# Optimization experiments

Measured on AMD Instinct MI355X. Metric: run time of the kernel, lower is better.

The kernel has to match this reference:

```python
import jax, jax.numpy as jnp
import numpy as np
import math

B, N, HID, NH = 128, 512, 512, 8
DH = HID // NH  # d_heads = 64


def setup_inputs() -> dict:
    key = jax.random.key(0)
    ks = jax.random.split(key, 8)
    s = 0.05  # keep logits in a sane range
    h = jax.random.normal(ks[0], (B, N, HID), dtype=jnp.float32)
    lengths = jax.random.randint(ks[1], (B,), 1, N + 1, dtype=jnp.int32)
    w_q = jax.random.normal(ks[2], (HID, HID), dtype=jnp.float32) * s
    w_k = jax.random.normal(ks[3], (HID, HID), dtype=jnp.float32) * s
    w_v = jax.random.normal(ks[4], (HID, HID), dtype=jnp.float32) * s
    w_o = jax.random.normal(ks[5], (HID, HID), dtype=jnp.float32) * s
    w_seed_w = jax.random.normal(ks[6], (HID, 1), dtype=jnp.float32) * s  # Linear(1, k*hidden), k=1
    w_seed_b = jax.random.normal(ks[7], (HID,), dtype=jnp.float32) * s
    seed_vec = jnp.ones((1,), dtype=jnp.float32)
    return {"h": h, "lengths": lengths, "w_q": w_q, "w_k": w_k, "w_v": w_v,
            "w_o": w_o, "w_seed_w": w_seed_w, "w_seed_b": w_seed_b, "seed_vec": seed_vec}


def reference(h, lengths, w_q, w_k, w_v, w_o, w_seed_w, w_seed_b, seed_vec):
    # PMA with k=1 seed query. norm_features=False.
    # query = w_seed(seed_vec), same for every graph in the batch.
    query = w_seed_w @ seed_vec + w_seed_b            # [HID]
    q = (w_q @ query).reshape(NH, DH)                 # [NH, DH] (Linear: x @ W.T == W @ x for vector)
    # NOTE: original code computes w_k(v) but never uses it in attention; output
    # depends only on q and v (e = q * v summed over d_heads). We skip the dead compute.
    v = (h @ w_v.T).reshape(B, N, NH, DH)             # [B, N, NH, DH]
    # logits: e[b,h,n] = <q[h], v[b,n,h]> / sqrt(DH)
    e = jnp.einsum("hd,bnhd->bhn", q, v) / math.sqrt(DH)
    valid = jnp.arange(N)[None, :] < lengths[:, None]  # [B, N] ragged mask
    e = jnp.where(valid[:, None, :], e, -jnp.inf)
    alpha = jax.nn.softmax(e, axis=-1)                # [B, NH, N]; padded cols -> 0
    out_h = jnp.einsum("bhn,bnhd->bhd", alpha, v)     # [B, NH, DH]
    out = out_h.reshape(B, HID) @ w_o.T               # [B*k, HID], packed (k=1)
    alpha_out = alpha[..., None]                      # [B, NH, N, 1] matching torch permute
    return out, alpha_out
```

## Files before the change

kernel.cpp:

```cpp
#include <hip/hip_runtime.h>
#include <math.h>

constexpr int B = 128, N = 512, HID = 512, NH = 8, DH = 64;

__global__ __launch_bounds__(256) void k1_qk(
    const float* __restrict__ w_q, const float* __restrict__ w_v,
    const float* __restrict__ w_sw, const float* __restrict__ w_sb,
    const float* __restrict__ seed, float* __restrict__ qk)
{
    __shared__ __align__(16) float query_s[HID];
    __shared__ float q_s[DH];
    __shared__ float red_s[4][64];
    const int t  = threadIdx.x;
    const int l  = t & 63;
    const int w  = t >> 6;
    const int h  = blockIdx.x >> 3;
    const int jc = blockIdx.x & 7;
    const float sv = seed[0];
    {
        const int j = t * 2;
        query_s[j]     = w_sw[j]     * sv + w_sb[j];
        query_s[j + 1] = w_sw[j + 1] * sv + w_sb[j + 1];
    }
    __syncthreads();
    {
        const float4 qa = *(const float4*)&query_s[l * 8];
        const float4 qb = *(const float4*)&query_s[l * 8 + 4];
        for (int i = 0; i < 16; ++i) {
            const int r = w * 16 + i;
            const float* row = w_q + (size_t)(h * DH + r) * HID + l * 8;
            const float4 a = *(const float4*)row;
            const float4 bx = *(const float4*)(row + 4);
            float acc = a.x * qa.x + a.y * qa.y + a.z * qa.z + a.w * qa.w
                      + bx.x * qb.x + bx.y * qb.y + bx.z * qb.z + bx.w * qb.w;
            #pragma unroll
            for (int off = 32; off; off >>= 1) acc += __shfl_xor(acc, off, 64);
            if (l == 0) q_s[r] = acc;
        }
    }
    __syncthreads();
    {
        const int j = jc * 64 + l;
        float acc = 0.f;
        #pragma unroll
        for (int i = 0; i < 16; ++i) {
            const int d = w * 16 + i;
            acc += q_s[d] * w_v[(size_t)(h * DH + d) * HID + j];
        }
        red_s[w][l] = acc;
    }
    __syncthreads();
    if (t < 64) {
        const float v = red_s[0][t] + red_s[1][t] + red_s[2][t] + red_s[3][t];
        qk[h * HID + jc * 64 + t] = v * 0.125f;
    }
}

__global__ __launch_bounds__(256) void kp_fused(
    const float* __restrict__ hbuf, const int* __restrict__ lengths,
    const float* __restrict__ qk, float* __restrict__ e_t,
    float* __restrict__ ctxp, float2* __restrict__ stats)
{
    __shared__ __align__(16) float rowbuf[16][HID];
    __shared__ float e_s[16][NH];
    __shared__ float p_s[16][NH];
    __shared__ float f_s[NH];

    const int t = threadIdx.x;
    const int l = t & 63;
    const int w = t >> 6;
    const int b = blockIdx.x >> 3;
    const int c = blockIdx.x & 7;
    const int n0 = c * 64;
    const int len = lengths[b];
    const int bc = b * 8 + c;

    if (n0 >= len) {
        if (t < NH) stats[bc * NH + t] = make_float2(-3.0e38f, 0.f);
        float4* cz = (float4*)(ctxp + (size_t)bc * NH * HID);
        const float4 z = {0.f, 0.f, 0.f, 0.f};
        #pragma unroll
        for (int i = 0; i < 4; ++i) cz[t * 4 + i] = z;
        return;
    }

    float4 qlo[NH], qhi[NH];
    #pragma unroll
    for (int hh = 0; hh < NH; ++hh) {
        qlo[hh] = *(const float4*)&qk[hh * HID + l * 4];
        qhi[hh] = *(const float4*)&qk[hh * HID + 256 + l * 4];
    }

    const float* hb = hbuf + (size_t)b * N * HID;
    const int hh_out = ((l & 1) << 2) | (l & 2) | ((l >> 2) & 1);
    const int hh_m = t >> 5;
    const int cg   = t & 31;
    const int li   = l & 31;
    const int hh_s = w + ((l >> 5) << 2);

    float m_run = -3.0e38f, s_run = 0.f;
    float4 acc0 = {0,0,0,0}, acc1 = {0,0,0,0}, acc2 = {0,0,0,0}, acc3 = {0,0,0,0};

    #pragma unroll 1
    for (int sc = 0; sc < 4; ++sc) {
        const int rn0 = n0 + sc * 16;
        const int nv = min(16, len - rn0);

        #pragma unroll
        for (int k = 0; k < 4; ++k) {
            const int rl = w + 4 * k;
            if (rl < nv) {
                const int rn = rn0 + rl;
                const float* row = hb + (size_t)rn * HID;
                const float4 h0 = *(const float4*)(row + l * 4);
                const float4 h1 = *(const float4*)(row + 256 + l * 4);
                *(float4*)&rowbuf[rl][l * 4] = h0;
                *(float4*)&rowbuf[rl][256 + l * 4] = h1;
                float v[NH];
                #pragma unroll
                for (int hh = 0; hh < NH; ++hh)
                    v[hh] = h0.x * qlo[hh].x + h0.y * qlo[hh].y
                          + h0.z * qlo[hh].z + h0.w * qlo[hh].w
                          + h1.x * qhi[hh].x + h1.y * qhi[hh].y
                          + h1.z * qhi[hh].z + h1.w * qhi[hh].w;
                #pragma unroll
                for (int i = 0; i < 4; ++i) {
                    const float ax = __shfl_xor(v[i], 1, 64);
                    const float bx = __shfl_xor(v[i + 4], 1, 64);
                    v[i] = (l & 1) ? (v[i + 4] + bx) : (v[i] + ax);
                }
                #pragma unroll
                for (int i = 0; i < 2; ++i) {
                    const float ax = __shfl_xor(v[i], 2, 64);
                    const float bx = __shfl_xor(v[i + 2], 2, 64);
                    v[i] = (l & 2) ? (v[i + 2] + bx) : (v[i] + ax);
                }
                {
                    const float ax = __shfl_xor(v[0], 4, 64);
                    const float bx = __shfl_xor(v[1], 4, 64);
                    v[0] = (l & 4) ? (v[1] + bx) : (v[0] + ax);
                }
                v[0] += __shfl_xor(v[0], 8, 64);
                v[0] += __shfl_xor(v[0], 16, 64);
                v[0] += __shfl_xor(v[0], 32, 64);
                if (l < 8) {
                    e_t[((size_t)b * N + rn) * NH + hh_out] = v[0];
                    e_s[rl][hh_out] = v[0];
                }
            }
        }
        __syncthreads();

        {
            const float e = (li < nv) ? e_s[li][hh_s] : -3.0e38f;
            float m_sub = e;
            m_sub = fmaxf(m_sub, __shfl_xor(m_sub, 1, 64));
            m_sub = fmaxf(m_sub, __shfl_xor(m_sub, 2, 64));
            m_sub = fmaxf(m_sub, __shfl_xor(m_sub, 4, 64));
            m_sub = fmaxf(m_sub, __shfl_xor(m_sub, 8, 64));
            const float m_new = fmaxf(m_run, m_sub);
            const float p = (li < nv) ? __expf(e - m_new) : 0.f;
            float s_sub = p;
            s_sub += __shfl_xor(s_sub, 1, 64);
            s_sub += __shfl_xor(s_sub, 2, 64);
            s_sub += __shfl_xor(s_sub, 4, 64);
            s_sub += __shfl_xor(s_sub, 8, 64);
            const float f = __expf(m_run - m_new);
            s_run = s_run * f + s_sub;
            m_run = m_new;
            if (li < nv) p_s[li][hh_s] = p;
            if (li == 0) f_s[hh_s] = f;
        }
        __syncthreads();

        {
            const float f = f_s[hh_m];
            acc0.x *= f; acc0.y *= f; acc0.z *= f; acc0.w *= f;
            acc1.x *= f; acc1.y *= f; acc1.z *= f; acc1.w *= f;
            acc2.x *= f; acc2.y *= f; acc2.z *= f; acc2.w *= f;
            acc3.x *= f; acc3.y *= f; acc3.z *= f; acc3.w *= f;
            for (int rl = 0; rl < nv; ++rl) {
                const float p = p_s[rl][hh_m];
                const float4 r0 = *(const float4*)&rowbuf[rl][cg * 4];
                const float4 r1 = *(const float4*)&rowbuf[rl][128 + cg * 4];
                const float4 r2 = *(const float4*)&rowbuf[rl][256 + cg * 4];
                const float4 r3 = *(const float4*)&rowbuf[rl][384 + cg * 4];
                acc0.x = fmaf(p, r0.x, acc0.x); acc0.y = fmaf(p, r0.y, acc0.y);
                acc0.z = fmaf(p, r0.z, acc0.z); acc0.w = fmaf(p, r0.w, acc0.w);
                acc1.x = fmaf(p, r1.x, acc1.x); acc1.y = fmaf(p, r1.y, acc1.y);
                acc1.z = fmaf(p, r1.z, acc1.z); acc1.w = fmaf(p, r1.w, acc1.w);
                acc2.x = fmaf(p, r2.x, acc2.x); acc2.y = fmaf(p, r2.y, acc2.y);
                acc2.z = fmaf(p, r2.z, acc2.z); acc2.w = fmaf(p, r2.w, acc2.w);
                acc3.x = fmaf(p, r3.x, acc3.x); acc3.y = fmaf(p, r3.y, acc3.y);
                acc3.z = fmaf(p, r3.z, acc3.z); acc3.w = fmaf(p, r3.w, acc3.w);
            }
        }
        __syncthreads();
    }

    if (li == 0) stats[bc * NH + hh_s] = make_float2(m_run, s_run);
    float* cp = ctxp + ((size_t)bc * NH + hh_m) * HID + cg * 4;
    *(float4*)(cp + 0)   = acc0;
    *(float4*)(cp + 128) = acc1;
    *(float4*)(cp + 256) = acc2;
    *(float4*)(cp + 384) = acc3;
}

__global__ __launch_bounds__(256) void ka_alpha(
    const int* __restrict__ lengths, const float* __restrict__ e_t,
    const float2* __restrict__ stats, float* __restrict__ alpha)
{
    __shared__ float m_l[NH], rs_l[NH];
    __shared__ float al_s[NH][N];
    const int t = threadIdx.x;
    const int b = blockIdx.x;
    const int len = lengths[b];
    if (t < NH) {
        float M = -3.0e38f;
        #pragma unroll
        for (int cc = 0; cc < 8; ++cc)
            M = fmaxf(M, stats[(b * 8 + cc) * NH + t].x);
        float S = 0.f;
        #pragma unroll
        for (int cc = 0; cc < 8; ++cc) {
            const float2 ms = stats[(b * 8 + cc) * NH + t];
            S += ms.y * __expf(ms.x - M);
        }
        m_l[t] = M;
        rs_l[t] = 1.f / S;
    }
    __syncthreads();
    const float* eb = e_t + (size_t)b * N * NH;
    #pragma unroll
    for (int k = 0; k < 16; ++k) {
        const int flat = k * 256 + t;
        const int n = flat >> 3;
        const int hh = flat & 7;
        const float e = eb[flat];
        al_s[hh][n] = (n < len) ? __expf(e - m_l[hh]) * rs_l[hh] : 0.f;
    }
    __syncthreads();
    float* ab = alpha + (size_t)b * NH * N;
    const float* af = (const float*)al_s;
    #pragma unroll
    for (int k = 0; k < 16; ++k) {
        const int flat = k * 256 + t;
        ab[flat] = af[flat];
    }
}

__global__ __launch_bounds__(256) void kd1_oh(
    const float* __restrict__ ctxp, const float2* __restrict__ stats,
    const float* __restrict__ w_v, float* __restrict__ oh)
{
    __shared__ __align__(16) float ctx_s[16][HID];
    __shared__ float w_s[16][8];
    const int t  = threadIdx.x;
    const int ht = blockIdx.x & 7;
    const int bt = blockIdx.x >> 3;

    if (t < 16) {
        const int bb = bt * 16 + t;
        float m_c[8], s_c[8];
        float M = -3.0e38f;
        #pragma unroll
        for (int cc = 0; cc < 8; ++cc) {
            const float2 ms = stats[(bb * 8 + cc) * NH + ht];
            m_c[cc] = ms.x; s_c[cc] = ms.y;
            M = fmaxf(M, ms.x);
        }
        float S = 0.f;
        #pragma unroll
        for (int cc = 0; cc < 8; ++cc) S += s_c[cc] * __expf(m_c[cc] - M);
        const float rS = 1.f / S;
        #pragma unroll
        for (int cc = 0; cc < 8; ++cc) w_s[t][cc] = __expf(m_c[cc] - M) * rS;
    }
    __syncthreads();

    for (int idx = t; idx < 16 * 128; idx += 256) {
        const int bb_l = idx >> 7;
        const int j4   = idx & 127;
        const int bb   = bt * 16 + bb_l;
        const float* p0 = ctxp + ((size_t)(bb * 8) * NH + ht) * HID + j4 * 4;
        float4 s = {0.f, 0.f, 0.f, 0.f};
        #pragma unroll
        for (int cc = 0; cc < 8; ++cc) {
            const float wcc = w_s[bb_l][cc];
            const float4 v = *(const float4*)(p0 + (size_t)cc * NH * HID);
            s.x = fmaf(wcc, v.x, s.x); s.y = fmaf(wcc, v.y, s.y);
            s.z = fmaf(wcc, v.z, s.z); s.w = fmaf(wcc, v.w, s.w);
        }
        *(float4*)&ctx_s[bb_l][j4 * 4] = s;
    }
    __syncthreads();

    const int d  = t & 63;
    const int bs = t >> 6;
    const int p  = ht * 64 + d;
    const float* wrow = w_v + (size_t)p * HID;
    float acc[4] = {0.f, 0.f, 0.f, 0.f};
    for (int j = 0; j < HID; j += 4) {
        const float4 wv = *(const float4*)(wrow + j);
        #pragma unroll
        for (int bi = 0; bi < 4; ++bi) {
            const float4 cv = *(const float4*)&ctx_s[bs * 4 + bi][j];
            acc[bi] += wv.x * cv.x + wv.y * cv.y + wv.z * cv.z + wv.w * cv.w;
        }
    }
    #pragma unroll
    for (int bi = 0; bi < 4; ++bi) {
        const int bb = bt * 16 + bs * 4 + bi;
        oh[(size_t)bb * HID + p] = acc[bi];
    }
}

__global__ __launch_bounds__(256) void kd2_out(
    const float* __restrict__ oh, const float* __restrict__ w_o,
    float* __restrict__ out)
{
    __shared__ __align__(16) float oh_s[16][HID];
    const int t  = threadIdx.x;
    const int it = blockIdx.x & 7;
    const int bt = blockIdx.x >> 3;

    for (int idx = t; idx < 16 * 128; idx += 256) {
        const int bb_l = idx >> 7;
        const int j4   = idx & 127;
        const int bb   = bt * 16 + bb_l;
        *(float4*)&oh_s[bb_l][j4 * 4] =
            *(const float4*)&oh[(size_t)bb * HID + j4 * 4];
    }
    __syncthreads();

    const int d  = t & 63;
    const int bs = t >> 6;
    const int i  = it * 64 + d;
    const float* wrow = w_o + (size_t)i * HID;
    float acc[4] = {0.f, 0.f, 0.f, 0.f};
    for (int j = 0; j < HID; j += 4) {
        const float4 wv = *(const float4*)(wrow + j);
        #pragma unroll
        for (int bi = 0; bi < 4; ++bi) {
            const float4 ov = *(const float4*)&oh_s[bs * 4 + bi][j];
            acc[bi] += wv.x * ov.x + wv.y * ov.y + wv.z * ov.z + wv.w * ov.w;
        }
    }
    #pragma unroll
    for (int bi = 0; bi < 4; ++bi) {
        const int bb = bt * 16 + bs * 4 + bi;
        out[(size_t)bb * HID + i] = acc[bi];
    }
}

extern "C" void kernel_launch(void* const* d_in, const int* in_sizes, int n_in,
                              void* d_out, int out_size, void* d_ws, size_t ws_size,
                              hipStream_t stream) {
    const float* h     = (const float*)d_in[0];
    const int*   lens  = (const int*)  d_in[1];
    const float* w_q   = (const float*)d_in[2];
    const float* w_v   = (const float*)d_in[4];
    const float* w_o   = (const float*)d_in[5];
    const float* w_sw  = (const float*)d_in[6];
    const float* w_sb  = (const float*)d_in[7];
    const float* seed  = (const float*)d_in[8];

    float* out   = (float*)d_out;
    float* alpha = out + (size_t)B * HID;

    float* ws    = (float*)d_ws;
    float* qk    = ws;
    float* e_t   = qk + NH * HID;
    float* ctxp  = e_t + (size_t)B * N * NH;
    float* statf = ctxp + (size_t)B * 8 * NH * HID;
    float* oh    = statf + (size_t)B * 8 * NH * 2;

    hipLaunchKernelGGL(k1_qk,    dim3(64),    dim3(256), 0, stream,
                       w_q, w_v, w_sw, w_sb, seed, qk);
    hipLaunchKernelGGL(kp_fused, dim3(B * 8), dim3(256), 0, stream,
                       h, lens, qk, e_t, ctxp, (float2*)statf);
    hipLaunchKernelGGL(ka_alpha, dim3(B),     dim3(256), 0, stream,
                       lens, e_t, (const float2*)statf, alpha);
    hipLaunchKernelGGL(kd1_oh,   dim3(64),    dim3(256), 0, stream,
                       ctxp, (const float2*)statf, w_v, oh);
    hipLaunchKernelGGL(kd2_out,  dim3(64),    dim3(256), 0, stream,
                       oh, w_o, out);
}
```

Before: 286.4 us.

## Replace staged softmax-pooling with per-wave register online softmax, fewer chunks

The main kernel no longer stages rows in shared memory with block barriers per 16-row subchunk. Each wave now streams its own rows and keeps a per-head online-softmax state and context accumulators in registers. The four wave partials are merged through shared memory at the end. Sequence chunks per graph drop from 8 to 4, so there are fewer blocks and less partial-context traffic to the combine kernel. In exchange, register pressure rises sharply (64 accumulator floats plus q vectors), which may spill or lower occupancy, and fewer, longer blocks are less balanced across ragged lengths.

```diff
diff --git a/kernel.cpp b/kernel.cpp
--- a/kernel.cpp
+++ b/kernel.cpp
@@ -2,6 +2,8 @@
 #include <math.h>
 
 constexpr int B = 128, N = 512, HID = 512, NH = 8, DH = 64;
+constexpr int CH = 4;
+constexpr int CROWS = N / CH;
 
 __global__ __launch_bounds__(256) void k1_qk(
     const float* __restrict__ w_q, const float* __restrict__ w_v,
@@ -56,31 +58,31 @@
     }
 }
 
-__global__ __launch_bounds__(256) void kp_fused(
+__global__ __launch_bounds__(256, 2) void kf_flash(
     const float* __restrict__ hbuf, const int* __restrict__ lengths,
     const float* __restrict__ qk, float* __restrict__ e_t,
     float* __restrict__ ctxp, float2* __restrict__ stats)
 {
-    __shared__ __align__(16) float rowbuf[16][HID];
-    __shared__ float e_s[16][NH];
-    __shared__ float p_s[16][NH];
-    __shared__ float f_s[NH];
+    __shared__ __align__(16) float part[4][NH][HID];
+    __shared__ float2 ms_s[4][NH];
+    __shared__ float fct[4][NH];
+    __shared__ float mc_s[NH];
 
     const int t = threadIdx.x;
     const int l = t & 63;
     const int w = t >> 6;
-    const int b = blockIdx.x >> 3;
-    const int c = blockIdx.x & 7;
-    const int n0 = c * 64;
+    const int b = blockIdx.x >> 2;
+    const int c = blockIdx.x & 3;
+    const int n0 = c * CROWS;
     const int len = lengths[b];
-    const int bc = b * 8 + c;
+    const int bc = b * CH + c;
 
     if (n0 >= len) {
         if (t < NH) stats[bc * NH + t] = make_float2(-3.0e38f, 0.f);
         float4* cz = (float4*)(ctxp + (size_t)bc * NH * HID);
         const float4 z = {0.f, 0.f, 0.f, 0.f};
         #pragma unroll
-        for (int i = 0; i < 4; ++i) cz[t * 4 + i] = z;
+        for (int i = 0; i < 4; ++i) cz[i * 256 + t] = z;
         return;
     }
 
@@ -92,118 +94,136 @@
     }
 
     const float* hb = hbuf + (size_t)b * N * HID;
+    const int nmax = min(n0 + CROWS, len);
     const int hh_out = ((l & 1) << 2) | (l & 2) | ((l >> 2) & 1);
-    const int hh_m = t >> 5;
-    const int cg   = t & 31;
-    const int li   = l & 31;
-    const int hh_s = w + ((l >> 5) << 2);
-
-    float m_run = -3.0e38f, s_run = 0.f;
-    float4 acc0 = {0,0,0,0}, acc1 = {0,0,0,0}, acc2 = {0,0,0,0}, acc3 = {0,0,0,0};
-
-    #pragma unroll 1
-    for (int sc = 0; sc < 4; ++sc) {
-        const int rn0 = n0 + sc * 16;
-        const int nv = min(16, len - rn0);
-
-        #pragma unroll
-        for (int k = 0; k < 4; ++k) {
-            const int rl = w + 4 * k;
-            if (rl < nv) {
-                const int rn = rn0 + rl;
-                const float* row = hb + (size_t)rn * HID;
-                const float4 h0 = *(const float4*)(row + l * 4);
-                const float4 h1 = *(const float4*)(row + 256 + l * 4);
-                *(float4*)&rowbuf[rl][l * 4] = h0;
-                *(float4*)&rowbuf[rl][256 + l * 4] = h1;
-                float v[NH];
-                #pragma unroll
-                for (int hh = 0; hh < NH; ++hh)
-                    v[hh] = h0.x * qlo[hh].x + h0.y * qlo[hh].y
-                          + h0.z * qlo[hh].z + h0.w * qlo[hh].w
-                          + h1.x * qhi[hh].x + h1.y * qhi[hh].y
-                          + h1.z * qhi[hh].z + h1.w * qhi[hh].w;
-                #pragma unroll
-                for (int i = 0; i < 4; ++i) {
-                    const float ax = __shfl_xor(v[i], 1, 64);
-                    const float bx = __shfl_xor(v[i + 4], 1, 64);
-                    v[i] = (l & 1) ? (v[i + 4] + bx) : (v[i] + ax);
-                }
-                #pragma unroll
-                for (int i = 0; i < 2; ++i) {
-                    const float ax = __shfl_xor(v[i], 2, 64);
-                    const float bx = __shfl_xor(v[i + 2], 2, 64);
-                    v[i] = (l & 2) ? (v[i + 2] + bx) : (v[i] + ax);
-                }
-                {
-                    const float ax = __shfl_xor(v[0], 4, 64);
-                    const float bx = __shfl_xor(v[1], 4, 64);
-                    v[0] = (l & 4) ? (v[1] + bx) : (v[0] + ax);
-                }
-                v[0] += __shfl_xor(v[0], 8, 64);
-                v[0] += __shfl_xor(v[0], 16, 64);
-                v[0] += __shfl_xor(v[0], 32, 64);
-                if (l < 8) {
-                    e_t[((size_t)b * N + rn) * NH + hh_out] = v[0];
-                    e_s[rl][hh_out] = v[0];
-                }
+
+    float m_run[NH], s_run[NH];
+    float4 acc0[NH], acc1[NH];
+    #pragma unroll
+    for (int hh = 0; hh < NH; ++hh) {
+        m_run[hh] = -3.0e38f; s_run[hh] = 0.f;
+        acc0[hh] = make_float4(0.f, 0.f, 0.f, 0.f);
+        acc1[hh] = make_float4(0.f, 0.f, 0.f, 0.f);
+    }
+
+    for (int n = n0 + w; n < nmax; n += 4) {
+        const float* row = hb + (size_t)n * HID;
+        const float4 h0 = *(const float4*)(row + l * 4);
+        const float4 h1 = *(const float4*)(row + 256 + l * 4);
+        float v[NH];
+        #pragma unroll
+        for (int hh = 0; hh < NH; ++hh)
+            v[hh] = h0.x * qlo[hh].x + h0.y * qlo[hh].y
+                  + h0.z * qlo[hh].z + h0.w * qlo[hh].w
+                  + h1.x * qhi[hh].x + h1.y * qhi[hh].y
+                  + h1.z * qhi[hh].z + h1.w * qhi[hh].w;
+        #pragma unroll
+        for (int i = 0; i < 4; ++i) {
+            const float ax = __shfl_xor(v[i], 1, 64);
+            const float bx = __shfl_xor(v[i + 4], 1, 64);
+            v[i] = (l & 1) ? (v[i + 4] + bx) : (v[i] + ax);
+        }
+        #pragma unroll
+        for (int i = 0; i < 2; ++i) {
+            const float ax = __shfl_xor(v[i], 2, 64);
+            const float bx = __shfl_xor(v[i + 2], 2, 64);
+            v[i] = (l & 2) ? (v[i + 2] + bx) : (v[i] + ax);
+        }
+        {
+            const float ax = __shfl_xor(v[0], 4, 64);
+            const float bx = __shfl_xor(v[1], 4, 64);
+            v[0] = (l & 4) ? (v[1] + bx) : (v[0] + ax);
+        }
+        v[0] += __shfl_xor(v[0], 8, 64);
+        v[0] += __shfl_xor(v[0], 16, 64);
+        v[0] += __shfl_xor(v[0], 32, 64);
+        if (l < 8)
+            e_t[((size_t)b * N + n) * NH + hh_out] = v[0];
+
+        float e[NH];
+        e[0] = __shfl(v[0], 0, 64); e[1] = __shfl(v[0], 4, 64);
+        e[2] = __shfl(v[0], 2, 64); e[3] = __shfl(v[0], 6, 64);
+        e[4] = __shfl(v[0], 1, 64); e[5] = __shfl(v[0], 5, 64);
+        e[6] = __shfl(v[0], 3, 64); e[7] = __shfl(v[0], 7, 64);
+
+        bool bump = false;
+        #pragma unroll
+        for (int hh = 0; hh < NH; ++hh) bump = bump || (e[hh] > m_run[hh]);
+        if (bump) {
+            #pragma unroll
+            for (int hh = 0; hh < NH; ++hh) {
+                const float mn = fmaxf(m_run[hh], e[hh]);
+                const float f  = __expf(m_run[hh] - mn);
+                s_run[hh] *= f;
+                acc0[hh].x *= f; acc0[hh].y *= f; acc0[hh].z *= f; acc0[hh].w *= f;
+                acc1[hh].x *= f; acc1[hh].y *= f; acc1[hh].z *= f; acc1[hh].w *= f;
+                m_run[hh] = mn;
             }
         }
-        __syncthreads();
-
-        {
-            const float e = (li < nv) ? e_s[li][hh_s] : -3.0e38f;
-            float m_sub = e;
-            m_sub = fmaxf(m_sub, __shfl_xor(m_sub, 1, 64));
-            m_sub = fmaxf(m_sub, __shfl_xor(m_sub, 2, 64));
-            m_sub = fmaxf(m_sub, __shfl_xor(m_sub, 4, 64));
-            m_sub = fmaxf(m_sub, __shfl_xor(m_sub, 8, 64));
-            const float m_new = fmaxf(m_run, m_sub);
-            const float p = (li < nv) ? __expf(e - m_new) : 0.f;
-            float s_sub = p;
-            s_sub += __shfl_xor(s_sub, 1, 64);
-            s_sub += __shfl_xor(s_sub, 2, 64);
-            s_sub += __shfl_xor(s_sub, 4, 64);
-            s_sub += __shfl_xor(s_sub, 8, 64);
-            const float f = __expf(m_run - m_new);
-            s_run = s_run * f + s_sub;
-            m_run = m_new;
-            if (li < nv) p_s[li][hh_s] = p;
-            if (li == 0) f_s[hh_s] = f;
-        }
-        __syncthreads();
-
-        {
-            const float f = f_s[hh_m];
-            acc0.x *= f; acc0.y *= f; acc0.z *= f; acc0.w *= f;
-            acc1.x *= f; acc1.y *= f; acc1.z *= f; acc1.w *= f;
-            acc2.x *= f; acc2.y *= f; acc2.z *= f; acc2.w *= f;
-            acc3.x *= f; acc3.y *= f; acc3.z *= f; acc3.w *= f;
-            for (int rl = 0; rl < nv; ++rl) {
-                const float p = p_s[rl][hh_m];
-                const float4 r0 = *(const float4*)&rowbuf[rl][cg * 4];
-                const float4 r1 = *(const float4*)&rowbuf[rl][128 + cg * 4];
-                const float4 r2 = *(const float4*)&rowbuf[rl][256 + cg * 4];
-                const float4 r3 = *(const float4*)&rowbuf[rl][384 + cg * 4];
-                acc0.x = fmaf(p, r0.x, acc0.x); acc0.y = fmaf(p, r0.y, acc0.y);
-                acc0.z = fmaf(p, r0.z, acc0.z); acc0.w = fmaf(p, r0.w, acc0.w);
-                acc1.x = fmaf(p, r1.x, acc1.x); acc1.y = fmaf(p, r1.y, acc1.y);
-                acc1.z = fmaf(p, r1.z, acc1.z); acc1.w = fmaf(p, r1.w, acc1.w);
-                acc2.x = fmaf(p, r2.x, acc2.x); acc2.y = fmaf(p, r2.y, acc2.y);
-                acc2.z = fmaf(p, r2.z, acc2.z); acc2.w = fmaf(p, r2.w, acc2.w);
-                acc3.x = fmaf(p, r3.x, acc3.x); acc3.y = fmaf(p, r3.y, acc3.y);
-                acc3.z = fmaf(p, r3.z, acc3.z); acc3.w = fmaf(p, r3.w, acc3.w);
-            }
-        }
-        __syncthreads();
-    }
-
-    if (li == 0) stats[bc * NH + hh_s] = make_float2(m_run, s_run);
-    float* cp = ctxp + ((size_t)bc * NH + hh_m) * HID + cg * 4;
-    *(float4*)(cp + 0)   = acc0;
-    *(float4*)(cp + 128) = acc1;
-    *(float4*)(cp + 256) = acc2;
-    *(float4*)(cp + 384) = acc3;
+        #pragma unroll
+        for (int hh = 0; hh < NH; ++hh) {
+            const float p = __expf(e[hh] - m_run[hh]);
+            s_run[hh] += p;
+            acc0[hh].x = fmaf(p, h0.x, acc0[hh].x);
+            acc0[hh].y = fmaf(p, h0.y, acc0[hh].y);
+            acc0[hh].z = fmaf(p, h0.z, acc0[hh].z);
+            acc0[hh].w = fmaf(p, h0.w, acc0[hh].w);
+            acc1[hh].x = fmaf(p, h1.x, acc1[hh].x);
+            acc1[hh].y = fmaf(p, h1.y, acc1[hh].y);
+            acc1[hh].z = fmaf(p, h1.z, acc1[hh].z);
+            acc1[hh].w = fmaf(p, h1.w, acc1[hh].w);
+        }
+    }
+
+    #pragma unroll
+    for (int hh = 0; hh < NH; ++hh) {
+        *(float4*)&part[w][hh][l * 4]       = acc0[hh];
+        *(float4*)&part[w][hh][256 + l * 4] = acc1[hh];
+    }
+    if (l == 0) {
+        #pragma unroll
+        for (int hh = 0; hh < NH; ++hh)
+            ms_s[w][hh] = make_float2(m_run[hh], s_run[hh]);
+    }
+    __syncthreads();
+    if (t < NH) {
+        float mc = -3.0e38f;
+        #pragma unroll
+        for (int ww = 0; ww < 4; ++ww) mc = fmaxf(mc, ms_s[ww][t].x);
+        float sc = 0.f;
+        #pragma unroll
+        for (int ww = 0; ww < 4; ++ww)
+            sc += ms_s[ww][t].y * __expf(ms_s[ww][t].x - mc);
+        stats[bc * NH + t] = make_float2(mc, sc);
+        mc_s[t] = mc;
+    }
+    __syncthreads();
+    if (t < 32) {
+        const int ww = t >> 3, hh = t & 7;
+        fct[ww][hh] = __expf(ms_s[ww][hh].x - mc_s[hh]);
+    }
+    __syncthreads();
+    {
+        const int hh_m = t >> 5;
+        const int cg   = t & 31;
+        const float f0 = fct[0][hh_m], f1 = fct[1][hh_m];
+        const float f2 = fct[2][hh_m], f3 = fct[3][hh_m];
+        float* cp = ctxp + ((size_t)bc * NH + hh_m) * HID + cg * 4;
+        #pragma unroll
+        for (int q = 0; q < 4; ++q) {
+            const int col = cg * 4 + q * 128;
+            const float4 r0 = *(const float4*)&part[0][hh_m][col];
+            const float4 r1 = *(const float4*)&part[1][hh_m][col];
+            const float4 r2 = *(const float4*)&part[2][hh_m][col];
+            const float4 r3 = *(const float4*)&part[3][hh_m][col];
+            float4 o;
+            o.x = f0 * r0.x + f1 * r1.x + f2 * r2.x + f3 * r3.x;
+            o.y = f0 * r0.y + f1 * r1.y + f2 * r2.y + f3 * r3.y;
+            o.z = f0 * r0.z + f1 * r1.z + f2 * r2.z + f3 * r3.z;
+            o.w = f0 * r0.w + f1 * r1.w + f2 * r2.w + f3 * r3.w;
+            *(float4*)(cp + q * 128) = o;
+        }
+    }
 }
 
 __global__ __launch_bounds__(256) void ka_alpha(
@@ -218,12 +238,12 @@
     if (t < NH) {
         float M = -3.0e38f;
         #pragma unroll
-        for (int cc = 0; cc < 8; ++cc)
-            M = fmaxf(M, stats[(b * 8 + cc) * NH + t].x);
+        for (int cc = 0; cc < CH; ++cc)
+            M = fmaxf(M, stats[(b * CH + cc) * NH + t].x);
         float S = 0.f;
         #pragma unroll
-        for (int cc = 0; cc < 8; ++cc) {
-            const float2 ms = stats[(b * 8 + cc) * NH + t];
+        for (int cc = 0; cc < CH; ++cc) {
+            const float2 ms = stats[(b * CH + cc) * NH + t];
             S += ms.y * __expf(ms.x - M);
         }
         m_l[t] = M;
@@ -254,27 +274,27 @@
     const float* __restrict__ w_v, float* __restrict__ oh)
 {
     __shared__ __align__(16) float ctx_s[16][HID];
-    __shared__ float w_s[16][8];
+    __shared__ float w_s[16][CH];
     const int t  = threadIdx.x;
     const int ht = blockIdx.x & 7;
     const int bt = blockIdx.x >> 3;
 
     if (t < 16) {
         const int bb = bt * 16 + t;
-        float m_c[8], s_c[8];
+        float m_c[CH], s_c[CH];
         float M = -3.0e38f;
         #pragma unroll
-        for (int cc = 0; cc < 8; ++cc) {
-            const float2 ms = stats[(bb * 8 + cc) * NH + ht];
+        for (int cc = 0; cc < CH; ++cc) {
+            const float2 ms = stats[(bb * CH + cc) * NH + ht];
             m_c[cc] = ms.x; s_c[cc] = ms.y;
             M = fmaxf(M, ms.x);
         }
         float S = 0.f;
         #pragma unroll
-        for (int cc = 0; cc < 8; ++cc) S += s_c[cc] * __expf(m_c[cc] - M);
+        for (int cc = 0; cc < CH; ++cc) S += s_c[cc] * __expf(m_c[cc] - M);
         const float rS = 1.f / S;
         #pragma unroll
-        for (int cc = 0; cc < 8; ++cc) w_s[t][cc] = __expf(m_c[cc] - M) * rS;
+        for (int cc = 0; cc < CH; ++cc) w_s[t][cc] = __expf(m_c[cc] - M) * rS;
     }
     __syncthreads();
 
@@ -282,10 +302,10 @@
         const int bb_l = idx >> 7;
         const int j4   = idx & 127;
         const int bb   = bt * 16 + bb_l;
-        const float* p0 = ctxp + ((size_t)(bb * 8) * NH + ht) * HID + j4 * 4;
+        const float* p0 = ctxp + ((size_t)(bb * CH) * NH + ht) * HID + j4 * 4;
         float4 s = {0.f, 0.f, 0.f, 0.f};
         #pragma unroll
-        for (int cc = 0; cc < 8; ++cc) {
+        for (int cc = 0; cc < CH; ++cc) {
             const float wcc = w_s[bb_l][cc];
             const float4 v = *(const float4*)(p0 + (size_t)cc * NH * HID);
             s.x = fmaf(wcc, v.x, s.x); s.y = fmaf(wcc, v.y, s.y);
@@ -372,17 +392,17 @@
     float* qk    = ws;
     float* e_t   = qk + NH * HID;
     float* ctxp  = e_t + (size_t)B * N * NH;
-    float* statf = ctxp + (size_t)B * 8 * NH * HID;
-    float* oh    = statf + (size_t)B * 8 * NH * 2;
-
-    hipLaunchKernelGGL(k1_qk,    dim3(64),    dim3(256), 0, stream,
+    float* statf = ctxp + (size_t)B * CH * NH * HID;
+    float* oh    = statf + (size_t)B * CH * NH * 2;
+
+    hipLaunchKernelGGL(k1_qk,    dim3(64),     dim3(256), 0, stream,
                        w_q, w_v, w_sw, w_sb, seed, qk);
-    hipLaunchKernelGGL(kp_fused, dim3(B * 8), dim3(256), 0, stream,
+    hipLaunchKernelGGL(kf_flash, dim3(B * CH), dim3(256), 0, stream,
                        h, lens, qk, e_t, ctxp, (float2*)statf);
-    hipLaunchKernelGGL(ka_alpha, dim3(B),     dim3(256), 0, stream,
+    hipLaunchKernelGGL(ka_alpha, dim3(B),      dim3(256), 0, stream,
                        lens, e_t, (const float2*)statf, alpha);
-    hipLaunchKernelGGL(kd1_oh,   dim3(64),    dim3(256), 0, stream,
+    hipLaunchKernelGGL(kd1_oh,   dim3(64),     dim3(256), 0, stream,
                        ctxp, (const float2*)statf, w_v, oh);
-    hipLaunchKernelGGL(kd2_out,  dim3(64),    dim3(256), 0, stream,
+    hipLaunchKernelGGL(kd2_out,  dim3(64),     dim3(256), 0, stream,
                        oh, w_o, out);
 }
```

Measured after the change: 284.1 us. No clear change (-0.8%).
